# Kernel optimization log

Measured on AMD Instinct MI355X. Metric: run time of the kernel, lower is better.

The kernel has to match this reference:

```python
import jax, jax.numpy as jnp
import numpy as np

B, N, D = 2, 8192, 2
CIN, COUT = 6, 3
WID = 64
DEPTH = 3
M1, M2 = 12, 12
G = 64            # latent grid is G x G
K = 16            # neighbors
EDGE_IN = WID + 3 * D + 1  # 71


def _gelu(x):
    return jax.nn.gelu(x, approximate=False)  # torch nn.GELU default = exact erf


def _mlp1(x, W1, b1, W2, b2):
    # MLP(depth=1): Linear -> GELU -> Linear
    return _gelu(x @ W1 + b1) @ W2 + b2


def _mlp2(x, W1, b1, W2, b2, W3, b3):
    # MLP(depth=2): Linear -> GELU -> Linear -> GELU -> Linear
    h = _gelu(x @ W1 + b1)
    h = _gelu(h @ W2 + b2)
    return h @ W3 + b3


def _local_integral(src_c, qry_c, src_f, W1, b1, W2, b2, W3, b3):
    # src_c (B,Ns,D), qry_c (B,Nq,D), src_f (B,Ns,C) -> (B,Nq,WID)
    d2 = (jnp.sum(qry_c * qry_c, -1)[:, :, None]
          + jnp.sum(src_c * src_c, -1)[:, None, :]
          - 2.0 * jnp.einsum('bmd,bnd->bmn', qry_c, src_c))
    dist = jnp.sqrt(jnp.clip(d2, 0.0))                    # (B,Nq,Ns)
    neg, idx = jax.lax.top_k(-dist, K)                    # ascending distances
    nn_dist = -neg                                        # (B,Nq,K)
    gather = jax.vmap(lambda a, i: a[i])
    nc = gather(src_c, idx)                               # (B,Nq,K,D)
    nf = gather(src_f, idx)                               # (B,Nq,K,C)
    q = jnp.broadcast_to(qry_c[:, :, None, :], nc.shape)  # (B,Nq,K,D)
    rel = q - nc
    edge = jnp.concatenate([q, nc, rel, nn_dist[..., None], nf], axis=-1)
    # sigma = lower median of farthest-neighbor distance (torch.median semantics)
    last = jnp.sort(nn_dist[..., -1].reshape(-1))
    sigma = jnp.maximum(last[(last.shape[0] - 1) // 2], 1e-6)
    w = jnp.exp(-nn_dist[..., None] / sigma)              # (B,Nq,K,1)
    v = _mlp2(edge, W1, b1, W2, b2, W3, b3)               # (B,Nq,K,WID)
    return jnp.sum(w * v, axis=2) / jnp.clip(jnp.sum(w, axis=2), 1e-6)


def _spectral2d(x, w1, w2):
    # x (B,C,H,W); w* real-packed complex weights (Ci,Co,M1,M2,2)
    Bx, _, H, W = x.shape
    xf = jnp.fft.rfft2(x)                                 # (B,C,H,W//2+1) complex
    W1c = w1[..., 0] + 1j * w1[..., 1]
    W2c = w2[..., 0] + 1j * w2[..., 1]
    out = jnp.zeros((Bx, W1c.shape[1], H, W // 2 + 1), jnp.complex64)
    out = out.at[:, :, :M1, :M2].set(jnp.einsum('bixy,ioxy->boxy', xf[:, :, :M1, :M2], W1c))
    out = out.at[:, :, -M1:, :M2].set(jnp.einsum('bixy,ioxy->boxy', xf[:, :, -M1:, :M2], W2c))
    return jnp.fft.irfft2(out, s=(H, W))


def _fno_block(x, w1, w2, pw_W, pw_b):
    y = _spectral2d(x, w1, w2) + jnp.einsum('bihw,oi->bohw', x, pw_W) + pw_b[None, :, None, None]
    mu = jnp.mean(y, axis=(-2, -1), keepdims=True)        # InstanceNorm2d, no affine
    var = jnp.var(y, axis=(-2, -1), keepdims=True)
    return _gelu((y - mu) / jnp.sqrt(var + 1e-5))


def _latent_grid():
    ax = jnp.linspace(-1.0, 1.0, G, dtype=jnp.float32)
    gx, gy = jnp.meshgrid(ax, ax, indexing='ij')
    return jnp.stack([gx, gy], axis=-1).reshape(1, G * G, D)


def setup_inputs() -> dict:
    key = jax.random.key(0)
    ks = jax.random.split(key, 32)
    u = lambda k, sh, s: jax.random.uniform(k, sh, jnp.float32, -s, s)
    inp = {
        'coords': 2.0 * jax.random.uniform(ks[0], (B, N, D), jnp.float32) - 1.0,
        'features': jax.random.normal(ks[1], (B, N, CIN), jnp.float32),
        'lift_W1': u(ks[2], (CIN, WID), CIN ** -0.5), 'lift_b1': jnp.zeros((WID,), jnp.float32),
        'lift_W2': u(ks[3], (WID, WID), WID ** -0.5), 'lift_b2': jnp.zeros((WID,), jnp.float32),
        'gin_W1': u(ks[4], (EDGE_IN, WID), EDGE_IN ** -0.5), 'gin_b1': jnp.zeros((WID,), jnp.float32),
        'gin_W2': u(ks[5], (WID, WID), WID ** -0.5), 'gin_b2': jnp.zeros((WID,), jnp.float32),
        'gin_W3': u(ks[6], (WID, WID), WID ** -0.5), 'gin_b3': jnp.zeros((WID,), jnp.float32),
        'spec1': (1.0 / (WID * WID)) * jax.random.uniform(ks[7], (DEPTH, WID, WID, M1, M2, 2), jnp.float32),
        'spec2': (1.0 / (WID * WID)) * jax.random.uniform(ks[8], (DEPTH, WID, WID, M1, M2, 2), jnp.float32),
        'pw_W': u(ks[9], (DEPTH, WID, WID), WID ** -0.5),
        'pw_b': jnp.zeros((DEPTH, WID), jnp.float32),
        'gout_W1': u(ks[10], (EDGE_IN, WID), EDGE_IN ** -0.5), 'gout_b1': jnp.zeros((WID,), jnp.float32),
        'gout_W2': u(ks[11], (WID, WID), WID ** -0.5), 'gout_b2': jnp.zeros((WID,), jnp.float32),
        'gout_W3': u(ks[12], (WID, WID), WID ** -0.5), 'gout_b3': jnp.zeros((WID,), jnp.float32),
        'proj_W1': u(ks[13], (WID, WID), WID ** -0.5), 'proj_b1': jnp.zeros((WID,), jnp.float32),
        'proj_W2': u(ks[14], (WID, COUT), WID ** -0.5), 'proj_b2': jnp.zeros((COUT,), jnp.float32),
    }
    return inp


def reference(coords, features, lift_W1, lift_b1, lift_W2, lift_b2,
              gin_W1, gin_b1, gin_W2, gin_b2, gin_W3, gin_b3,
              spec1, spec2, pw_W, pw_b,
              gout_W1, gout_b1, gout_W2, gout_b2, gout_W3, gout_b3,
              proj_W1, proj_b1, proj_W2, proj_b2):
    grid = jnp.broadcast_to(_latent_grid(), (coords.shape[0], G * G, D))
    # lift node features
    feat = _mlp1(features, lift_W1, lift_b1, lift_W2, lift_b2)          # (B,N,WID)
    # GNO: points -> latent grid
    g = _local_integral(coords, grid, feat, gin_W1, gin_b1, gin_W2, gin_b2, gin_W3, gin_b3)
    x = g.reshape(-1, G, G, WID).transpose(0, 3, 1, 2)                  # (B,WID,G,G)
    for d in range(DEPTH):
        x = _fno_block(x, spec1[d], spec2[d], pw_W[d], pw_b[d])
    g = x.transpose(0, 2, 3, 1).reshape(-1, G * G, WID)                 # (B,G*G,WID)
    # GNO: latent grid -> points
    y = _local_integral(grid, coords, g, gout_W1, gout_b1, gout_W2, gout_b2, gout_W3, gout_b3)
    return _mlp1(y, proj_W1, proj_b1, proj_W2, proj_b2)                 # (B,N,COUT)
```

## Files before the change

kernel.cpp:

```cpp
#include <hip/hip_runtime.h>
#include <math.h>

#define B_ 2
#define N_ 8192
#define G_ 64
#define NG 4096
#define WID_ 64
#define K_ 16
#define CIN_ 6
#define COUT_ 3
#define PI_ 3.14159265358979323846

typedef unsigned long long u64k;
typedef __attribute__((ext_vector_type(8))) short bf16x8;
typedef __attribute__((ext_vector_type(16))) float f32x16;

__device__ __forceinline__ float gelu_f(float x) {
    float u = fabsf(x) * 0.70710678118654752440f;
    float t = __builtin_amdgcn_rcpf(fmaf(0.3275911f, u, 1.0f));
    float p = fmaf(fmaf(fmaf(fmaf(1.061405429f, t, -1.453152027f), t, 1.421413741f),
                        t, -0.284496736f), t, 0.254829592f) * t;
    float e = __expf(-u * u);
    float erfc_u = p * e;
    float phi = (x >= 0.f) ? fmaf(-0.5f, erfc_u, 1.0f) : (0.5f * erfc_u);
    return x * phi;
}
__device__ __forceinline__ int cellof(float v) {
    int c = (int)floorf((v + 1.0f) * 32.0f);
    return min(63, max(0, c));
}
__device__ __forceinline__ u64k umin64(u64k a, u64k b) { return a < b ? a : b; }
__device__ __forceinline__ u64k umax64(u64k a, u64k b) { return a < b ? b : a; }
__device__ __forceinline__ u64k shflxor64(u64k v, int m) {
    return (u64k)__shfl_xor((long long)v, m, 64);
}
__device__ __forceinline__ void bsort64(u64k& key, int lane) {
#pragma unroll
    for (int sz = 2; sz <= 64; sz <<= 1) {
#pragma unroll
        for (int j = sz >> 1; j >= 1; j >>= 1) {
            u64k o = shflxor64(key, j);
            bool keep_min = ((lane & j) == 0) == ((lane & sz) == 0);
            key = keep_min ? umin64(key, o) : umax64(key, o);
        }
    }
}
__device__ __forceinline__ void bmerge_into(u64k& R, u64k key, int lane) {
    u64k o = shflxor64(key, 63);
    u64k L = umin64(R, o);
#pragma unroll
    for (int j = 32; j >= 1; j >>= 1) {
        u64k t = shflxor64(L, j);
        L = ((lane & j) == 0) ? umin64(L, t) : umax64(L, t);
    }
    R = L;
}
__device__ __forceinline__ void cvt8v(float4 a, float4 b, bf16x8& hv, bf16x8& lv) {
    float v[8] = {a.x, a.y, a.z, a.w, b.x, b.y, b.z, b.w};
#pragma unroll
    for (int i = 0; i < 8; i++) {
        unsigned u = __float_as_uint(v[i]);
        unsigned r = (u + 0x8000u) & 0xffff0000u;
        hv[i] = (short)(r >> 16);
        float lo = v[i] - __uint_as_float(r);
        lv[i] = (short)(__float_as_uint(lo) >> 16);
    }
}
__device__ __forceinline__ bf16x8 ldfrag(const short* __restrict__ WB, int f, int lane) {
    return *(const bf16x8*)(WB + ((long)f * 64 + lane) * 8);
}
struct Frag4 { bf16x8 h0, l0, h1, l1; };
__device__ __forceinline__ Frag4 ldfrag4(const short* __restrict__ WB, int base, int nk,
                                         int kc, int lane) {
    Frag4 f;
    f.h0 = ldfrag(WB, base + (0 * nk + kc) * 2 + 0, lane);
    f.l0 = ldfrag(WB, base + (0 * nk + kc) * 2 + 1, lane);
    f.h1 = ldfrag(WB, base + (1 * nk + kc) * 2 + 0, lane);
    f.l1 = ldfrag(WB, base + (1 * nk + kc) * 2 + 1, lane);
    return f;
}

__global__ void __launch_bounds__(256) k_prep(
    const float* __restrict__ fin, const float* __restrict__ lW1,
    const float* __restrict__ lb1, const float* __restrict__ lW2,
    const float* __restrict__ lb2, float* __restrict__ fout,
    const float* __restrict__ W1a, const float* __restrict__ W2a,
    const float* __restrict__ W3a, short* __restrict__ WBa,
    const float* __restrict__ W1b, const float* __restrict__ W2b,
    const float* __restrict__ W3b, short* __restrict__ WBb,
    float4* __restrict__ gp, int* __restrict__ bins) {
    __shared__ float xr[4][8];
    __shared__ __align__(16) float h[4][64];
    int blk = blockIdx.x;
    if (blk < 4096) {
        int ql = threadIdx.x >> 6, j = threadIdx.x & 63;
        int node = blk * 4 + ql;
        if (j < CIN_) xr[ql][j] = fin[node * CIN_ + j];
        __syncthreads();
        float a = lb1[j];
#pragma unroll
        for (int i = 0; i < CIN_; i++) a = fmaf(xr[ql][i], lW1[i * 64 + j], a);
        h[ql][j] = gelu_f(a);
        __syncthreads();
        float a2 = lb2[j];
        for (int k = 0; k < 64; k += 4) {
            float w0 = lW2[(k + 0) * 64 + j], w1 = lW2[(k + 1) * 64 + j];
            float w2 = lW2[(k + 2) * 64 + j], w3 = lW2[(k + 3) * 64 + j];
            const float4 hv = *(const float4*)&h[ql][k];
            a2 = fmaf(hv.x, w0, fmaf(hv.y, w1, fmaf(hv.z, w2, fmaf(hv.w, w3, a2))));
        }
        fout[node * 64 + j] = a2;
    } else if (blk < 4122) {
        int t = (blk - 4096) * 256 + threadIdx.x;
        if (t >= 6656) return;
        int setb = (t >= 3328);
        int tt = t - (setb ? 3328 : 0);
        const float* W1s = setb ? W1b : W1a;
        const float* W2s = setb ? W2b : W2a;
        const float* W3s = setb ? W3b : W3a;
        short* WB = setb ? WBb : WBa;
        int f = tt >> 6, lane = tt & 63;
        const float* W; int hh, nt, kc, l1 = 0;
        if (f < 20)      { W = W1s; int r = f;      hh = r & 1; r >>= 1; nt = r / 5; kc = r % 5; l1 = 1; }
        else if (f < 36) { W = W2s; int r = f - 20; hh = r & 1; r >>= 1; nt = r / 4; kc = r % 4; }
        else             { W = W3s; int r = f - 36; hh = r & 1; r >>= 1; nt = r / 4; kc = r % 4; }
        int col = nt * 32 + (lane & 31);
        bf16x8 out;
#pragma unroll
        for (int i = 0; i < 8; i++) {
            int k = kc * 16 + (lane >> 5) * 8 + i;
            float w = 0.f;
            if (l1) {
                if (k < 7) w = W[k * 64 + col];
                else if (k >= 8 && k < 72) w = W[(k - 1) * 64 + col];
            } else {
                w = W[k * 64 + col];
            }
            unsigned u = __float_as_uint(w);
            unsigned hi = (u + 0x7fffu + ((u >> 16) & 1u)) & 0xffff0000u;
            float lo = w - __uint_as_float(hi);
            unsigned ul = __float_as_uint(lo);
            unsigned lr = ul + 0x7fffu + ((ul >> 16) & 1u);
            out[i] = hh ? (short)(lr >> 16) : (short)(hi >> 16);
        }
        *(bf16x8*)(WB + ((long)f * 64 + lane) * 8) = out;
    } else if (blk < 4138) {
        int t = (blk - 4122) * 256 + threadIdx.x;
        int i = t >> 6, j = t & 63;
        double st = 2.0 / 63.0;
        float gx = (i == 63) ? 1.0f : (float)(-1.0 + st * (double)i);
        float gy = (j == 63) ? 1.0f : (float)(-1.0 + st * (double)j);
        float s2 = __fadd_rn(__fmul_rn(gx, gx), __fmul_rn(gy, gy));
        gp[t] = make_float4(gx, gy, s2, 0.f);
    } else {
        int t = (blk - 4138) * 256 + threadIdx.x;
        bins[t] = 0;
    }
}

__global__ void k_bincount(const float2* __restrict__ coords, int* __restrict__ cnt) {
    int t = blockIdx.x * blockDim.x + threadIdx.x;
    if (t >= B_ * N_) return;
    float2 c = coords[t];
    int b = t >> 13;
    int cell = cellof(c.x) * 64 + cellof(c.y);
    atomicAdd(&cnt[b * 4096 + cell], 1);
}
__global__ void k_binscan(const int* __restrict__ cnt, int* __restrict__ offs) {
    int b = blockIdx.x, t = threadIdx.x;
    __shared__ int part[16];
    int4 v = ((const int4*)(cnt + b * 4096))[t];
    int sum = v.x + v.y + v.z + v.w;
    int lane = t & 63, wv = t >> 6;
    int ws = sum;
#pragma unroll
    for (int o = 1; o < 64; o <<= 1) {
        int u = __shfl_up(ws, o, 64);
        if (lane >= o) ws += u;
    }
    if (lane == 63) part[wv] = ws;
    __syncthreads();
    int base = 0;
#pragma unroll
    for (int k = 0; k < 16; k++) base += (k < wv) ? part[k] : 0;
    int incl = base + ws, excl = incl - sum;
    int* ob = offs + b * 4097;
    ob[4 * t] = excl; ob[4 * t + 1] = excl + v.x;
    ob[4 * t + 2] = excl + v.x + v.y; ob[4 * t + 3] = excl + v.x + v.y + v.z;
    if (t == 1023) ob[4096] = incl;
}
__global__ void k_binscatter(const float2* __restrict__ coords, const int* __restrict__ offs,
                             int* __restrict__ fill, float4* __restrict__ srt) {
    int t = blockIdx.x * blockDim.x + threadIdx.x;
    if (t >= B_ * N_) return;
    float2 c = coords[t];
    int b = t >> 13, n = t & 8191;
    int cell = cellof(c.x) * 64 + cellof(c.y);
    int pos = offs[b * 4097 + cell] + atomicAdd(&fill[b * 4096 + cell], 1);
    float s2 = __fadd_rn(__fmul_rn(c.x, c.x), __fmul_rn(c.y, c.y));
    srt[b * N_ + pos] = make_float4(c.x, c.y, s2, __int_as_float(n));
}

__global__ void __launch_bounds__(256) k_knn(
    const float4* __restrict__ gp, const float4* __restrict__ srt,
    const int* __restrict__ offs, const float2* __restrict__ coords,
    int* __restrict__ oidx_in, float* __restrict__ odist_in, float* __restrict__ lastd_in,
    int* __restrict__ oidx_out, float* __restrict__ odist_out, float* __restrict__ lastd_out) {
    int lane = threadIdx.x & 63;
    if (blockIdx.x < 2048) {
        int w = (blockIdx.x * blockDim.x + threadIdx.x) >> 6;
        int b = w >> 12, p = w & 4095;
        float4 q = gp[p];
        float qx = q.x, qy = q.y, q2 = q.z;
        int cqx = cellof(qx), cqy = cellof(qy);
        const float4* S = srt + b * N_;
        const int* OF = offs + b * 4097;

        u64k R = ~0ull;
        u64k pend = ~0ull;
        int fill = 0;

        auto flush = [&]() {
            bsort64(pend, lane);
            bmerge_into(R, pend, lane);
            pend = ~0ull;
            fill = 0;
        };
        auto feed = [&](int s0, int s1) {
            int cnt = s1 - s0;
            while (cnt > 0) {
                int take = min(cnt, 64 - fill);
                int t = lane - fill;
                if (t >= 0 && t < take) {
                    float4 sp = S[s0 + t];
                    float dot = __fadd_rn(__fmul_rn(qx, sp.x), __fmul_rn(qy, sp.y));
                    float d2 = __fsub_rn(__fadd_rn(q2, sp.z), 2.0f * dot);
                    d2 = fmaxf(d2, 0.0f);
                    pend = ((u64k)__float_as_uint(d2) << 32) | (unsigned)__float_as_int(sp.w);
                }
                fill += take; s0 += take; cnt -= take;
                if (fill == 64) flush();
            }
        };

        {
            int xa = max(cqx - 2, 0), xb = min(cqx + 2, 63);
            int ya = max(cqy - 2, 0), yb = min(cqy + 2, 63);
            for (int cx = xa; cx <= xb; cx++) feed(OF[cx * 64 + ya], OF[cx * 64 + yb + 1]);
        }
        int r = 2;
        while (true) {
            if (fill) flush();
            u64k T = (u64k)__shfl((long long)R, 15, 64);
            float d16 = __uint_as_float((unsigned)(T >> 32));
            float bm = (float)r * 0.03125f;
            if (d16 < bm * bm - 1e-5f) break;
            if (cqx - r <= 0 && cqx + r >= 63 && cqy - r <= 0 && cqy + r >= 63) break;
            r++;
            int ya = max(cqy - r, 0), yb = min(cqy + r, 63);
            if (cqx - r >= 0)  { int c0 = (cqx - r) * 64; feed(OF[c0 + ya], OF[c0 + yb + 1]); }
            if (cqx + r <= 63) { int c0 = (cqx + r) * 64; feed(OF[c0 + ya], OF[c0 + yb + 1]); }
            int xa2 = max(cqx - r + 1, 0), xb2 = min(cqx + r - 1, 63);
            for (int cx = xa2; cx <= xb2; cx++) {
                if (cqy - r >= 0)  { int cc = cx * 64 + cqy - r; feed(OF[cc], OF[cc + 1]); }
                if (cqy + r <= 63) { int cc = cx * 64 + cqy + r; feed(OF[cc], OF[cc + 1]); }
            }
        }
        if (lane < 16) {
            float d2 = __uint_as_float((unsigned)(R >> 32));
            float d = sqrtf(d2);
            oidx_in[w * 16 + lane] = (int)(unsigned)(R & 0xffffffffu);
            odist_in[w * 16 + lane] = d;
            if (lane == 15) lastd_in[w] = d;
        }
    } else {
        int w = ((blockIdx.x - 2048) * blockDim.x + threadIdx.x) >> 6;
        float2 c = coords[w];
        float qx = c.x, qy = c.y;
        float q2 = __fadd_rn(__fmul_rn(qx, qx), __fmul_rn(qy, qy));
        int i0 = (int)floorf((qx + 1.0f) * 31.5f);
        int j0 = (int)floorf((qy + 1.0f) * 31.5f);
        int li = min(max(i0 - 3, 0), 56);
        int lj = min(max(j0 - 3, 0), 56);
        int p = (li + (lane >> 3)) * 64 + (lj + (lane & 7));
        float4 sp = gp[p];
        float dot = __fadd_rn(__fmul_rn(qx, sp.x), __fmul_rn(qy, sp.y));
        float d2 = fmaxf(__fsub_rn(__fadd_rn(q2, sp.z), 2.0f * dot), 0.0f);
        u64k key = ((u64k)__float_as_uint(d2) << 32) | (unsigned)p;
        bsort64(key, lane);
        if (lane < 16) {
            float dd = sqrtf(__uint_as_float((unsigned)(key >> 32)));
            oidx_out[w * 16 + lane] = (int)(unsigned)(key & 0xffffffffu);
            odist_out[w * 16 + lane] = dd;
            if (lane == 15) lastd_out[w] = dd;
        }
    }
}

__global__ void __launch_bounds__(1024) k_median2(
    const float* __restrict__ vin, const float* __restrict__ vout,
    float* __restrict__ sig_in, float* __restrict__ sig_out) {
    const float* vals = blockIdx.x ? vout : vin;
    int n = blockIdx.x ? (B_ * N_) : (B_ * NG);
    float* sig = blockIdx.x ? sig_out : sig_in;
    __shared__ int wred[2][16];
    int tid = threadIdx.x;
    int lane = tid & 63, wv = tid >> 6;
    int cnt_per = n >> 10;
    unsigned v[16];
    for (int i = 0; i < cnt_per; i++) v[i] = __float_as_uint(vals[tid + (i << 10)]);
    int r = (n - 1) >> 1;
    unsigned prefix = 0;
    for (int bit = 31; bit >= 0; bit--) {
        unsigned cand = prefix | (1u << bit);
        int c = 0;
        for (int i = 0; i < cnt_per; i++) c += (v[i] < cand) ? 1 : 0;
        for (int o = 32; o >= 1; o >>= 1) c += __shfl_down(c, o, 64);
        int buf = bit & 1;
        if (lane == 0) wred[buf][wv] = c;
        __syncthreads();
        int tot = 0;
#pragma unroll
        for (int k = 0; k < 16; k++) tot += wred[buf][k];
        prefix = (tot <= r) ? cand : prefix;
    }
    if (tid == 0) *sig = fmaxf(__uint_as_float(prefix), 1e-6f);
}

template <int MODE>
__global__ void __launch_bounds__(128, 4) k_edge_mfma(
    const int* __restrict__ idxb, const float* __restrict__ distb,
    const float* __restrict__ sigp,
    const float2* __restrict__ coords, const float4* __restrict__ gp,
    const float* __restrict__ feats, const short* __restrict__ WB,
    const float* __restrict__ b1, const float* __restrict__ b2,
    const float* __restrict__ b3,
    float* __restrict__ outb) {
    constexpr int QSH  = (MODE == 0) ? 12 : 13;
    constexpr int QMSK = (MODE == 0) ? 4095 : 8191;
    constexpr long SR  = (MODE == 0) ? 8192 : 4096;
    __shared__ float X[2][2432];
    const int tid = threadIdx.x, wv = tid >> 6, lane = tid & 63;
    const int r31 = lane & 31, g = lane >> 5;
    const int qbase = (blockIdx.x * 2 + wv) * 2;
    const float sig = *sigp;
    float* X_ = X[wv];

    Frag4 cur = ldfrag4(WB, 0, 5, 0, lane);

    int si = 0; float wt = 0.f;
    if (lane < 32) {
        int q = lane >> 4, e = lane & 15;
        int gq = qbase + q;
        int b = gq >> QSH, p = gq & QMSK;
        si = idxb[gq * 16 + e];
        float d = distb[gq * 16 + e];
        wt = __expf(-d / sig);
        float qx, qy, sx, sy;
        if (MODE == 0) {
            float4 gv = gp[p]; qx = gv.x; qy = gv.y;
            float2 cc = coords[(long)b * SR + si]; sx = cc.x; sy = cc.y;
        } else {
            float2 cc = coords[gq]; qx = cc.x; qy = cc.y;
            float4 gv = gp[si]; sx = gv.x; sy = gv.y;
        }
        float* row = X_ + lane * 76;
        *(float4*)row       = make_float4(qx, qy, sx, sy);
        *(float4*)(row + 4) = make_float4(qx - sx, qy - sy, d, 0.f);
    }
    float swt = wt;
#pragma unroll
    for (int m = 1; m < 16; m <<= 1) swt += __shfl_xor(swt, m, 64);
    {
        float4 fv[8];
#pragma unroll
        for (int it = 0; it < 8; it++) {
            int slot = it * 64 + lane;
            int row = slot >> 4, f4 = slot & 15;
            int gq = qbase + (row >> 4);
            int b = gq >> QSH;
            int sr = __shfl(si, row, 64);
            fv[it] = *(const float4*)&feats[((long)b * SR + sr) * 64 + f4 * 4];
        }
#pragma unroll
        for (int it = 0; it < 8; it++) {
            int slot = it * 64 + lane;
            int row = slot >> 4, f4 = slot & 15;
            *(float4*)&X_[row * 76 + 8 + f4 * 4] = fv[it];
        }
    }

    f32x16 acc0, acc1;
    float4 xa, xb;
    {
        float bb0 = b1[r31], bb1 = b1[32 + r31];
#pragma unroll
        for (int i = 0; i < 16; i++) { acc0[i] = bb0; acc1[i] = bb1; }
        {
            const float* xp = &X_[r31 * 76 + g * 8];
            xa = *(const float4*)xp; xb = *(const float4*)(xp + 4);
        }
#pragma unroll
        for (int kc = 0; kc < 5; kc++) {
            Frag4 nxt = (kc < 4) ? ldfrag4(WB, 0, 5, kc + 1, lane)
                                 : ldfrag4(WB, 20, 4, 0, lane);
            bf16x8 ah, al;
            if (kc == 4 && g) {
#pragma unroll
                for (int i = 0; i < 8; i++) { ah[i] = 0; al[i] = 0; }
            } else {
                cvt8v(xa, xb, ah, al);
            }
            if (kc < 4 && (kc != 3 || g == 0)) {
                const float* xp = &X_[r31 * 76 + (kc + 1) * 16 + g * 8];
                xa = *(const float4*)xp; xb = *(const float4*)(xp + 4);
            }
            __builtin_amdgcn_s_setprio(1);
            acc0 = __builtin_amdgcn_mfma_f32_32x32x16_bf16(ah, cur.h0, acc0, 0, 0, 0);
            acc1 = __builtin_amdgcn_mfma_f32_32x32x16_bf16(ah, cur.h1, acc1, 0, 0, 0);
            acc0 = __builtin_amdgcn_mfma_f32_32x32x16_bf16(al, cur.h0, acc0, 0, 0, 0);
            acc1 = __builtin_amdgcn_mfma_f32_32x32x16_bf16(al, cur.h1, acc1, 0, 0, 0);
            acc0 = __builtin_amdgcn_mfma_f32_32x32x16_bf16(ah, cur.l0, acc0, 0, 0, 0);
            acc1 = __builtin_amdgcn_mfma_f32_32x32x16_bf16(ah, cur.l1, acc1, 0, 0, 0);
            __builtin_amdgcn_s_setprio(0);
            cur = nxt;
        }
    }
#pragma unroll
    for (int reg = 0; reg < 16; reg++) {
        int row = (reg & 3) + 8 * (reg >> 2) + 4 * g;
        X_[row * 76 + r31]      = gelu_f(acc0[reg]);
        X_[row * 76 + 32 + r31] = gelu_f(acc1[reg]);
    }
    {
        float bb0 = b2[r31], bb1 = b2[32 + r31];
#pragma unroll
        for (int i = 0; i < 16; i++) { acc0[i] = bb0; acc1[i] = bb1; }
        {
            const float* xp = &X_[r31 * 76 + g * 8];
            xa = *(const float4*)xp; xb = *(const float4*)(xp + 4);
        }
#pragma unroll
        for (int kc = 0; kc < 4; kc++) {
            Frag4 nxt = (kc < 3) ? ldfrag4(WB, 20, 4, kc + 1, lane)
                                 : ldfrag4(WB, 36, 4, 0, lane);
            bf16x8 ah, al;
            cvt8v(xa, xb, ah, al);
            if (kc < 3) {
                const float* xp = &X_[r31 * 76 + (kc + 1) * 16 + g * 8];
                xa = *(const float4*)xp; xb = *(const float4*)(xp + 4);
            }
            __builtin_amdgcn_s_setprio(1);
            acc0 = __builtin_amdgcn_mfma_f32_32x32x16_bf16(ah, cur.h0, acc0, 0, 0, 0);
            acc1 = __builtin_amdgcn_mfma_f32_32x32x16_bf16(ah, cur.h1, acc1, 0, 0, 0);
            acc0 = __builtin_amdgcn_mfma_f32_32x32x16_bf16(al, cur.h0, acc0, 0, 0, 0);
            acc1 = __builtin_amdgcn_mfma_f32_32x32x16_bf16(al, cur.h1, acc1, 0, 0, 0);
            acc0 = __builtin_amdgcn_mfma_f32_32x32x16_bf16(ah, cur.l0, acc0, 0, 0, 0);
            acc1 = __builtin_amdgcn_mfma_f32_32x32x16_bf16(ah, cur.l1, acc1, 0, 0, 0);
            __builtin_amdgcn_s_setprio(0);
            cur = nxt;
        }
    }
#pragma unroll
    for (int reg = 0; reg < 16; reg++) {
        int row = (reg & 3) + 8 * (reg >> 2) + 4 * g;
        X_[row * 76 + r31]      = gelu_f(acc0[reg]);
        X_[row * 76 + 32 + r31] = gelu_f(acc1[reg]);
    }
    {
        float bb0 = b3[r31], bb1 = b3[32 + r31];
#pragma unroll
        for (int i = 0; i < 16; i++) { acc0[i] = bb0; acc1[i] = bb1; }
        {
            const float* xp = &X_[r31 * 76 + g * 8];
            xa = *(const float4*)xp; xb = *(const float4*)(xp + 4);
        }
#pragma unroll
        for (int kc = 0; kc < 4; kc++) {
            Frag4 nxt = cur;
            if (kc < 3) nxt = ldfrag4(WB, 36, 4, kc + 1, lane);
            bf16x8 ah, al;
            cvt8v(xa, xb, ah, al);
            if (kc < 3) {
                const float* xp = &X_[r31 * 76 + (kc + 1) * 16 + g * 8];
                xa = *(const float4*)xp; xb = *(const float4*)(xp + 4);
            }
            __builtin_amdgcn_s_setprio(1);
            acc0 = __builtin_amdgcn_mfma_f32_32x32x16_bf16(ah, cur.h0, acc0, 0, 0, 0);
            acc1 = __builtin_amdgcn_mfma_f32_32x32x16_bf16(ah, cur.h1, acc1, 0, 0, 0);
            acc0 = __builtin_amdgcn_mfma_f32_32x32x16_bf16(al, cur.h0, acc0, 0, 0, 0);
            acc1 = __builtin_amdgcn_mfma_f32_32x32x16_bf16(al, cur.h1, acc1, 0, 0, 0);
            acc0 = __builtin_amdgcn_mfma_f32_32x32x16_bf16(ah, cur.l0, acc0, 0, 0, 0);
            acc1 = __builtin_amdgcn_mfma_f32_32x32x16_bf16(ah, cur.l1, acc1, 0, 0, 0);
            __builtin_amdgcn_s_setprio(0);
            cur = nxt;
        }
    }
    float wtv[16];
#pragma unroll
    for (int reg = 0; reg < 16; reg++)
        wtv[reg] = __shfl(wt, (reg & 3) + 8 * (reg >> 2) + 4 * g, 64);
    float s00 = 0.f, s01 = 0.f, s10 = 0.f, s11 = 0.f;
#pragma unroll
    for (int reg = 0; reg < 16; reg++) {
        if (reg < 8) { s00 = fmaf(wtv[reg], acc0[reg], s00); s01 = fmaf(wtv[reg], acc1[reg], s01); }
        else         { s10 = fmaf(wtv[reg], acc0[reg], s10); s11 = fmaf(wtv[reg], acc1[reg], s11); }
    }
    s00 += __shfl_xor(s00, 32, 64);
    s01 += __shfl_xor(s01, 32, 64);
    s10 += __shfl_xor(s10, 32, 64);
    s11 += __shfl_xor(s11, 32, 64);
    float sw0 = __shfl(swt, 0, 64), sw1 = __shfl(swt, 16, 64);
    if (g == 0) {
        float i0 = 1.0f / fmaxf(sw0, 1e-6f), i1 = 1.0f / fmaxf(sw1, 1e-6f);
        int gq0 = qbase, gq1 = qbase + 1;
        if (MODE == 0) {
            int b0 = gq0 >> QSH, p0 = gq0 & QMSK;
            int b1i = gq1 >> QSH, p1 = gq1 & QMSK;
            outb[((long)b0 * 64 + r31) * 4096 + p0]        = s00 * i0;
            outb[((long)b0 * 64 + 32 + r31) * 4096 + p0]   = s01 * i0;
            outb[((long)b1i * 64 + r31) * 4096 + p1]       = s10 * i1;
            outb[((long)b1i * 64 + 32 + r31) * 4096 + p1]  = s11 * i1;
        } else {
            outb[(long)gq0 * 64 + r31]      = s00 * i0;
            outb[(long)gq0 * 64 + 32 + r31] = s01 * i0;
            outb[(long)gq1 * 64 + r31]      = s10 * i1;
            outb[(long)gq1 * 64 + 32 + r31] = s11 * i1;
        }
    }
}

__global__ void k_transp(const float* __restrict__ src, float* __restrict__ dst, int R, int C) {
    __shared__ float t[32][33];
    int b = blockIdx.z;
    int c0 = blockIdx.x * 32, r0 = blockIdx.y * 32;
    int tx = threadIdx.x, ty0 = threadIdx.y;
    for (int yy = ty0; yy < 32; yy += 8) {
        int r = r0 + yy, c = c0 + tx;
        if (r < R && c < C) t[yy][tx] = src[((long)b * R + r) * C + c];
    }
    __syncthreads();
    for (int yy = ty0; yy < 32; yy += 8) {
        int c = c0 + yy, r = r0 + tx;
        if (r < R && c < C) dst[((long)b * C + c) * R + r] = t[tx][yy];
    }
}

__global__ void __launch_bounds__(384) k_f1(const float* __restrict__ x, float* __restrict__ Xh) {
    int blk = blockIdx.x >> 1;
    int chalf = blockIdx.x & 1;
    int tid = threadIdx.x;
    __shared__ __align__(16) float img[4096];
    __shared__ float Tre[64][6], Tim[64][6];
    __shared__ float cs[64], sn[64];
    if (tid < 64) {
        double a = (2.0 * PI_ / 64.0) * (double)tid;
        cs[tid] = (float)cos(a);
        sn[tid] = (float)sin(a);
    }
    for (int t = tid; t < 1024; t += 384)
        ((float4*)img)[t] = ((const float4*)(x + (long)blk * 4096))[t];
    __syncthreads();
    {
        int h = tid / 6, cl = tid - 6 * h;
        int c = chalf * 6 + cl;
        float cr = cs[c], sr = sn[c];
        float pr = 1.f, pi = 0.f;
        float re = 0.f, im = 0.f;
#pragma unroll 16
        for (int w = 0; w < 64; w++) {
            if (w == 32) {
                int k = (c * 32) & 63;
                pr = cs[k]; pi = sn[k];
            }
            float v = img[h * 64 + w];
            re = fmaf(v, pr, re);
            im = fmaf(-v, pi, im);
            float nr = pr * cr - pi * sr;
            pi = fmaf(pr, sr, pi * cr);
            pr = nr;
        }
        Tre[h][cl] = re; Tim[h][cl] = im;
    }
    __syncthreads();
    if (tid < 144) {
        int xx = tid / 6, cl = tid - 6 * xx;
        int r = (xx < 12) ? xx : (xx + 40);
        float cr = cs[r], sr = sn[r];
        float pr = 1.f, pi = 0.f;
        float re = 0.f, im = 0.f;
#pragma unroll 16
        for (int h = 0; h < 64; h++) {
            if (h == 32) {
                int k = (r * 32) & 63;
                pr = cs[k]; pi = sn[k];
            }
            float a = Tre[h][cl], bb = Tim[h][cl];
            re += a * pr + bb * pi;
            im += bb * pr - a * pi;
            float nr = pr * cr - pi * sr;
            pi = fmaf(pr, sr, pi * cr);
            pr = nr;
        }
        int m = xx * 12 + chalf * 6 + cl;
        Xh[((long)blk * 288 + m) * 2] = re;
        Xh[((long)blk * 288 + m) * 2 + 1] = im;
    }
}

__global__ void __launch_bounds__(320) k_f2(const float* __restrict__ Xh, const float* __restrict__ s1,
                                            const float* __restrict__ s2, float* __restrict__ Yh) {
    int bo = blockIdx.x;
    int b = bo >> 6, o = bo & 63;
    int m = threadIdx.x;
    if (m >= 288) return;
    int xx = m / 12, y = m - 12 * xx;
    const float* W; int xw;
    if (xx < 12) { W = s1; xw = xx; } else { W = s2; xw = xx - 12; }
    long wbase = (long)o * 288 + xw * 24 + y * 2;
    const float* Xb = Xh + ((long)b * 64) * 576;
    float re = 0.f, im = 0.f;
    for (int i = 0; i < 64; i++) {
        float2 wv = *(const float2*)&W[(long)i * 18432 + wbase];
        float2 xv = *(const float2*)&Xb[(long)i * 576 + m * 2];
        re += xv.x * wv.x - xv.y * wv.y;
        im += xv.x * wv.y + xv.y * wv.x;
    }
    float* Yb = Yh + (((long)b * 64 + o) * 288 + m) * 2;
    Yb[0] = re; Yb[1] = im;
}

__global__ void __launch_bounds__(1024) k_f3(const float* __restrict__ Yh, const float* __restrict__ x,
                                             const float* __restrict__ pwW, const float* __restrict__ pwb,
                                             float* __restrict__ xo) {
    int blk = blockIdx.x;
    int b = blk >> 6, o = blk & 63;
    int tid = threadIdx.x;
    __shared__ float yre[288], yim[288];
    __shared__ float Qre[64][12], Qim[64][12];
    __shared__ float cs[64], sn[64];
    __shared__ float red[16];
    if (tid < 64) {
        double a = (2.0 * PI_ / 64.0) * (double)tid;
        cs[tid] = (float)cos(a);
        sn[tid] = (float)sin(a);
    }
    if (tid < 288) {
        yre[tid] = Yh[((long)blk * 288 + tid) * 2];
        yim[tid] = Yh[((long)blk * 288 + tid) * 2 + 1];
    }
    __syncthreads();
    if (tid < 768) {
        int h = tid / 12, c = tid - 12 * h;
        float re = 0.f, im = 0.f;
#pragma unroll
        for (int xx = 0; xx < 24; xx++) {
            int r = (xx < 12) ? xx : (xx + 40);
            int k = (r * h) & 63;
            float wr = cs[k], wi = sn[k];
            float a = yre[xx * 12 + c], bb = yim[xx * 12 + c];
            re += a * wr - bb * wi;
            im += a * wi + bb * wr;
        }
        Qre[h][c] = re * (1.0f / 64.0f);
        Qim[h][c] = im * (1.0f / 64.0f);
    }
    __syncthreads();
    float bias = pwb[o];
    int h = tid >> 4;
    int w0 = (tid & 15) * 4;
    float sp0, sp1, sp2, sp3;
    {
        float base = Qre[h][0];
        sp0 = sp1 = sp2 = sp3 = base;
#pragma unroll
        for (int c = 1; c < 12; c++) {
            float qr = Qre[h][c], qi = Qim[h][c];
            int k0 = (c * w0) & 63, k1 = (c * (w0 + 1)) & 63;
            int k2 = (c * (w0 + 2)) & 63, k3 = (c * (w0 + 3)) & 63;
            sp0 += 2.0f * (qr * cs[k0] - qi * sn[k0]);
            sp1 += 2.0f * (qr * cs[k1] - qi * sn[k1]);
            sp2 += 2.0f * (qr * cs[k2] - qi * sn[k2]);
            sp3 += 2.0f * (qr * cs[k3] - qi * sn[k3]);
        }
    }
    float a0 = sp0 * (1.0f / 64.0f) + bias;
    float a1 = sp1 * (1.0f / 64.0f) + bias;
    float a2 = sp2 * (1.0f / 64.0f) + bias;
    float a3 = sp3 * (1.0f / 64.0f) + bias;
    const float* xb = x + ((long)b * 64) * 4096 + tid * 4;
    for (int i = 0; i < 64; i++) {
        float wv = pwW[o * 64 + i];
        const float4 xv = *(const float4*)(xb + (long)i * 4096);
        a0 = fmaf(xv.x, wv, a0);
        a1 = fmaf(xv.y, wv, a1);
        a2 = fmaf(xv.z, wv, a2);
        a3 = fmaf(xv.w, wv, a3);
    }
    float ssum = a0 + a1 + a2 + a3;
#pragma unroll
    for (int m = 1; m < 64; m <<= 1) ssum += __shfl_xor(ssum, m, 64);
    if ((tid & 63) == 0) red[tid >> 6] = ssum;
    __syncthreads();
    float mu = 0.f;
#pragma unroll
    for (int k = 0; k < 16; k++) mu += red[k];
    mu *= (1.0f / 4096.0f);
    __syncthreads();
    float d0 = a0 - mu, d1 = a1 - mu, d2 = a2 - mu, d3 = a3 - mu;
    float sq = d0 * d0 + d1 * d1 + d2 * d2 + d3 * d3;
#pragma unroll
    for (int m = 1; m < 64; m <<= 1) sq += __shfl_xor(sq, m, 64);
    if ((tid & 63) == 0) red[tid >> 6] = sq;
    __syncthreads();
    float var = 0.f;
#pragma unroll
    for (int k = 0; k < 16; k++) var += red[k];
    var *= (1.0f / 4096.0f);
    float inv = 1.0f / sqrtf(var + 1e-5f);
    float4 ov = make_float4(gelu_f(d0 * inv), gelu_f(d1 * inv), gelu_f(d2 * inv), gelu_f(d3 * inv));
    *(float4*)&xo[(long)blk * 4096 + tid * 4] = ov;
}

__global__ void __launch_bounds__(256) k_proj(
    const float* __restrict__ y, const float* __restrict__ W1, const float* __restrict__ b1,
    const float* __restrict__ W2, const float* __restrict__ b2, float* __restrict__ out) {
    __shared__ __align__(16) float yr[4][64];
    __shared__ float h[4][64];
    int ql = threadIdx.x >> 6, j = threadIdx.x & 63;
    long node = (long)blockIdx.x * 4 + ql;
    yr[ql][j] = y[node * 64 + j];
    __syncthreads();
    float a = b1[j];
    for (int k = 0; k < 64; k += 4) {
        float w0 = W1[(k + 0) * 64 + j], w1 = W1[(k + 1) * 64 + j];
        float w2 = W1[(k + 2) * 64 + j], w3 = W1[(k + 3) * 64 + j];
        const float4 hv = *(const float4*)&yr[ql][k];
        a = fmaf(hv.x, w0, fmaf(hv.y, w1, fmaf(hv.z, w2, fmaf(hv.w, w3, a))));
    }
    h[ql][j] = gelu_f(a);
    __syncthreads();
    if (j < 3) {
        float a2 = b2[j];
        for (int k = 0; k < 64; k++) a2 = fmaf(h[ql][k], W2[k * 3 + j], a2);
        out[node * 3 + j] = a2;
    }
}

extern "C" void kernel_launch(void* const* d_in, const int* in_sizes, int n_in,
                              void* d_out, int out_size, void* d_ws, size_t ws_size,
                              hipStream_t stream) {
    (void)in_sizes; (void)n_in; (void)out_size; (void)ws_size;
    const float* coords   = (const float*)d_in[0];
    const float* features = (const float*)d_in[1];
    const float* lift_W1 = (const float*)d_in[2];
    const float* lift_b1 = (const float*)d_in[3];
    const float* lift_W2 = (const float*)d_in[4];
    const float* lift_b2 = (const float*)d_in[5];
    const float* gin_W1 = (const float*)d_in[6];
    const float* gin_b1 = (const float*)d_in[7];
    const float* gin_W2 = (const float*)d_in[8];
    const float* gin_b2 = (const float*)d_in[9];
    const float* gin_W3 = (const float*)d_in[10];
    const float* gin_b3 = (const float*)d_in[11];
    const float* spec1 = (const float*)d_in[12];
    const float* spec2 = (const float*)d_in[13];
    const float* pw_W  = (const float*)d_in[14];
    const float* pw_b  = (const float*)d_in[15];
    const float* gout_W1 = (const float*)d_in[16];
    const float* gout_b1 = (const float*)d_in[17];
    const float* gout_W2 = (const float*)d_in[18];
    const float* gout_b2 = (const float*)d_in[19];
    const float* gout_W3 = (const float*)d_in[20];
    const float* gout_b3 = (const float*)d_in[21];
    const float* proj_W1 = (const float*)d_in[22];
    const float* proj_b1 = (const float*)d_in[23];
    const float* proj_W2 = (const float*)d_in[24];
    const float* proj_b2 = (const float*)d_in[25];

    char* ws = (char*)d_ws;
    size_t off = 0;
    auto alloc = [&](size_t bytes) -> char* {
        char* p = ws + off;
        off = (off + bytes + 255) & ~(size_t)255;
        return p;
    };
    float4* grid_pack = (float4*)alloc((size_t)NG * 16);
    float*  feat      = (float*)alloc((size_t)B_ * N_ * 64 * 4);
    int*    bin_cnt   = (int*)alloc((size_t)B_ * 4096 * 4);
    int*    bin_fill  = (int*)alloc((size_t)B_ * 4096 * 4);
    int*    bin_off   = (int*)alloc((size_t)B_ * 4097 * 4);
    float4* srt       = (float4*)alloc((size_t)B_ * N_ * 16);
    int*    idx_in    = (int*)alloc((size_t)B_ * NG * 16 * 4);
    float*  dist_in   = (float*)alloc((size_t)B_ * NG * 16 * 4);
    float*  lastd_in  = (float*)alloc((size_t)B_ * NG * 4);
    float*  sig_in    = (float*)alloc(256);
    float*  xb0       = (float*)alloc((size_t)B_ * 64 * NG * 4);
    float*  xb1       = (float*)alloc((size_t)B_ * 64 * NG * 4);
    float*  Xh        = (float*)alloc((size_t)B_ * 64 * 288 * 2 * 4);
    float*  Yh        = (float*)alloc((size_t)B_ * 64 * 288 * 2 * 4);
    float*  g2        = (float*)alloc((size_t)B_ * NG * 64 * 4);
    int*    idx_out   = (int*)alloc((size_t)B_ * N_ * 16 * 4);
    float*  dist_out  = (float*)alloc((size_t)B_ * N_ * 16 * 4);
    float*  lastd_out = (float*)alloc((size_t)B_ * N_ * 4);
    float*  sig_out   = (float*)alloc(256);
    float*  ybuf      = (float*)alloc((size_t)B_ * N_ * 64 * 4);
    short*  wb_in     = (short*)alloc((size_t)52 * 1024);
    short*  wb_out    = (short*)alloc((size_t)52 * 1024);

    k_prep<<<4202, 256, 0, stream>>>(features, lift_W1, lift_b1, lift_W2, lift_b2, feat,
                                     gin_W1, gin_W2, gin_W3, wb_in,
                                     gout_W1, gout_W2, gout_W3, wb_out,
                                     grid_pack, bin_cnt);
    k_bincount<<<(B_ * N_) / 256, 256, 0, stream>>>((const float2*)coords, bin_cnt);
    k_binscan<<<B_, 1024, 0, stream>>>(bin_cnt, bin_off);
    k_binscatter<<<(B_ * N_) / 256, 256, 0, stream>>>((const float2*)coords, bin_off, bin_fill, srt);
    k_knn<<<2048 + 4096, 256, 0, stream>>>(grid_pack, srt, bin_off, (const float2*)coords,
                                           idx_in, dist_in, lastd_in,
                                           idx_out, dist_out, lastd_out);
    k_median2<<<2, 1024, 0, stream>>>(lastd_in, lastd_out, sig_in, sig_out);
    k_edge_mfma<0><<<(B_ * NG) / 4, 128, 0, stream>>>(idx_in, dist_in, sig_in,
        (const float2*)coords, grid_pack, feat, wb_in,
        gin_b1, gin_b2, gin_b3, xb0);
    float* xc = xb0; float* xn = xb1;
    for (int d = 0; d < 3; d++) {
        k_f1<<<B_ * 64 * 2, 384, 0, stream>>>(xc, Xh);
        k_f2<<<B_ * 64, 320, 0, stream>>>(Xh, spec1 + (size_t)d * 1179648, spec2 + (size_t)d * 1179648, Yh);
        k_f3<<<B_ * 64, 1024, 0, stream>>>(Yh, xc, pw_W + (size_t)d * 4096, pw_b + (size_t)d * 64, xn);
        float* tmp = xc; xc = xn; xn = tmp;
    }
    {
        dim3 g(NG / 32, 64 / 32, B_); dim3 t(32, 8);
        k_transp<<<g, t, 0, stream>>>(xc, g2, 64, NG);
    }
    k_edge_mfma<1><<<(B_ * N_) / 4, 128, 0, stream>>>(idx_out, dist_out, sig_out,
        (const float2*)coords, grid_pack, g2, wb_out,
        gout_b1, gout_b2, gout_b3, ybuf);
    k_proj<<<(B_ * N_) / 4, 256, 0, stream>>>(ybuf, proj_W1, proj_b1, proj_W2, proj_b2, (float*)d_out);
}
```

Measured before the change: 363.0 us.

## Fuse spectral mixing, pointwise/norm and next-layer forward DFT; fold projection into edge kernel

Merges the spectral channel-mixing kernel into the inverse-DFT/pointwise kernel, splitting the 64-input-channel sum across two thread groups. For the first two FNO layers the same kernel also computes the next layer's truncated forward DFT from the result kept in shared memory, so the separate forward-DFT launch is needed only once. The output projection MLP moves into the epilogue of the second edge kernel, which removes the 64-wide intermediate buffer and one launch. The cost is much more shared memory per block and redundant weight loads in the fused kernels.

Result: faster. 336.9 us (median of 2 runs) (-7.2%).

```diff
diff --git a/kernel.cpp b/kernel.cpp
--- a/kernel.cpp
+++ b/kernel.cpp
@@ -335,6 +335,8 @@
     const float* __restrict__ feats, const short* __restrict__ WB,
     const float* __restrict__ b1, const float* __restrict__ b2,
     const float* __restrict__ b3,
+    const float* __restrict__ pW1, const float* __restrict__ pb1,
+    const float* __restrict__ pW2, const float* __restrict__ pb2,
     float* __restrict__ outb) {
     constexpr int QSH  = (MODE == 0) ? 12 : 13;
     constexpr int QMSK = (MODE == 0) ? 4095 : 8191;
@@ -511,21 +513,49 @@
     s10 += __shfl_xor(s10, 32, 64);
     s11 += __shfl_xor(s11, 32, 64);
     float sw0 = __shfl(swt, 0, 64), sw1 = __shfl(swt, 16, 64);
-    if (g == 0) {
-        float i0 = 1.0f / fmaxf(sw0, 1e-6f), i1 = 1.0f / fmaxf(sw1, 1e-6f);
-        int gq0 = qbase, gq1 = qbase + 1;
-        if (MODE == 0) {
+    float i0 = 1.0f / fmaxf(sw0, 1e-6f), i1 = 1.0f / fmaxf(sw1, 1e-6f);
+    int gq0 = qbase, gq1 = qbase + 1;
+    if (MODE == 0) {
+        if (g == 0) {
             int b0 = gq0 >> QSH, p0 = gq0 & QMSK;
             int b1i = gq1 >> QSH, p1 = gq1 & QMSK;
             outb[((long)b0 * 64 + r31) * 4096 + p0]        = s00 * i0;
             outb[((long)b0 * 64 + 32 + r31) * 4096 + p0]   = s01 * i0;
             outb[((long)b1i * 64 + r31) * 4096 + p1]       = s10 * i1;
             outb[((long)b1i * 64 + 32 + r31) * 4096 + p1]  = s11 * i1;
-        } else {
-            outb[(long)gq0 * 64 + r31]      = s00 * i0;
-            outb[(long)gq0 * 64 + 32 + r31] = s01 * i0;
-            outb[(long)gq1 * 64 + r31]      = s10 * i1;
-            outb[(long)gq1 * 64 + 32 + r31] = s11 * i1;
+        }
+    } else {
+        if (g == 0) {
+            X_[r31]       = s00 * i0;
+            X_[32 + r31]  = s01 * i0;
+            X_[64 + r31]  = s10 * i1;
+            X_[96 + r31]  = s11 * i1;
+        }
+        int j = lane;
+        float a0 = pb1[j], a1 = a0;
+        for (int k = 0; k < 64; k++) {
+            float w = pW1[k * 64 + j];
+            a0 = fmaf(X_[k], w, a0);
+            a1 = fmaf(X_[64 + k], w, a1);
+        }
+        float h0 = gelu_f(a0), h1 = gelu_f(a1);
+        float w20 = pW2[j * 3 + 0], w21 = pW2[j * 3 + 1], w22 = pW2[j * 3 + 2];
+        float p00 = h0 * w20, p01 = h0 * w21, p02 = h0 * w22;
+        float p10 = h1 * w20, p11 = h1 * w21, p12 = h1 * w22;
+#pragma unroll
+        for (int m = 1; m < 64; m <<= 1) {
+            p00 += __shfl_xor(p00, m, 64); p01 += __shfl_xor(p01, m, 64);
+            p02 += __shfl_xor(p02, m, 64);
+            p10 += __shfl_xor(p10, m, 64); p11 += __shfl_xor(p11, m, 64);
+            p12 += __shfl_xor(p12, m, 64);
+        }
+        if (lane == 0) {
+            outb[(long)gq0 * 3 + 0] = p00 + pb2[0];
+            outb[(long)gq0 * 3 + 1] = p01 + pb2[1];
+            outb[(long)gq0 * 3 + 2] = p02 + pb2[2];
+            outb[(long)gq1 * 3 + 0] = p10 + pb2[0];
+            outb[(long)gq1 * 3 + 1] = p11 + pb2[1];
+            outb[(long)gq1 * 3 + 2] = p12 + pb2[2];
         }
     }
 }
@@ -608,46 +638,48 @@
     }
 }
 
-__global__ void __launch_bounds__(320) k_f2(const float* __restrict__ Xh, const float* __restrict__ s1,
-                                            const float* __restrict__ s2, float* __restrict__ Yh) {
-    int bo = blockIdx.x;
-    int b = bo >> 6, o = bo & 63;
-    int m = threadIdx.x;
-    if (m >= 288) return;
-    int xx = m / 12, y = m - 12 * xx;
-    const float* W; int xw;
-    if (xx < 12) { W = s1; xw = xx; } else { W = s2; xw = xx - 12; }
-    long wbase = (long)o * 288 + xw * 24 + y * 2;
-    const float* Xb = Xh + ((long)b * 64) * 576;
-    float re = 0.f, im = 0.f;
-    for (int i = 0; i < 64; i++) {
-        float2 wv = *(const float2*)&W[(long)i * 18432 + wbase];
-        float2 xv = *(const float2*)&Xb[(long)i * 576 + m * 2];
-        re += xv.x * wv.x - xv.y * wv.y;
-        im += xv.x * wv.y + xv.y * wv.x;
-    }
-    float* Yb = Yh + (((long)b * 64 + o) * 288 + m) * 2;
-    Yb[0] = re; Yb[1] = im;
-}
-
-__global__ void __launch_bounds__(1024) k_f3(const float* __restrict__ Yh, const float* __restrict__ x,
-                                             const float* __restrict__ pwW, const float* __restrict__ pwb,
-                                             float* __restrict__ xo) {
+template <int RUN_DFT>
+__global__ void __launch_bounds__(1024) k_f23(
+    const float* __restrict__ Xh, const float* __restrict__ s1,
+    const float* __restrict__ s2, const float* __restrict__ x,
+    const float* __restrict__ pwW, const float* __restrict__ pwb,
+    float* __restrict__ xo, float* __restrict__ XhN) {
     int blk = blockIdx.x;
     int b = blk >> 6, o = blk & 63;
     int tid = threadIdx.x;
     __shared__ float yre[288], yim[288];
+    __shared__ float prr[576], pii[576];
     __shared__ float Qre[64][12], Qim[64][12];
     __shared__ float cs[64], sn[64];
     __shared__ float red[16];
+    __shared__ __align__(16) float img[4096];
+    __shared__ float Tre[64][12], Tim[64][12];
     if (tid < 64) {
         double a = (2.0 * PI_ / 64.0) * (double)tid;
         cs[tid] = (float)cos(a);
         sn[tid] = (float)sin(a);
     }
+    if (tid < 576) {
+        int grp = (tid >= 288) ? 1 : 0;
+        int m = tid - grp * 288;
+        int xx = m / 12, y = m - 12 * xx;
+        const float* W; int xw;
+        if (xx < 12) { W = s1; xw = xx; } else { W = s2; xw = xx - 12; }
+        long wbase = (long)o * 288 + xw * 24 + y * 2;
+        const float* Xb = Xh + ((long)b * 64) * 576;
+        float re = 0.f, im = 0.f;
+        for (int i = grp * 32; i < grp * 32 + 32; i++) {
+            float2 wv = *(const float2*)&W[(long)i * 18432 + wbase];
+            float2 xv = *(const float2*)&Xb[(long)i * 576 + m * 2];
+            re += xv.x * wv.x - xv.y * wv.y;
+            im += xv.x * wv.y + xv.y * wv.x;
+        }
+        prr[tid] = re; pii[tid] = im;
+    }
+    __syncthreads();
     if (tid < 288) {
-        yre[tid] = Yh[((long)blk * 288 + tid) * 2];
-        yim[tid] = Yh[((long)blk * 288 + tid) * 2 + 1];
+        yre[tid] = prr[tid] + prr[tid + 288];
+        yim[tid] = pii[tid] + pii[tid + 288];
     }
     __syncthreads();
     if (tid < 768) {
@@ -720,30 +752,52 @@
     float inv = 1.0f / sqrtf(var + 1e-5f);
     float4 ov = make_float4(gelu_f(d0 * inv), gelu_f(d1 * inv), gelu_f(d2 * inv), gelu_f(d3 * inv));
     *(float4*)&xo[(long)blk * 4096 + tid * 4] = ov;
-}
-
-__global__ void __launch_bounds__(256) k_proj(
-    const float* __restrict__ y, const float* __restrict__ W1, const float* __restrict__ b1,
-    const float* __restrict__ W2, const float* __restrict__ b2, float* __restrict__ out) {
-    __shared__ __align__(16) float yr[4][64];
-    __shared__ float h[4][64];
-    int ql = threadIdx.x >> 6, j = threadIdx.x & 63;
-    long node = (long)blockIdx.x * 4 + ql;
-    yr[ql][j] = y[node * 64 + j];
-    __syncthreads();
-    float a = b1[j];
-    for (int k = 0; k < 64; k += 4) {
-        float w0 = W1[(k + 0) * 64 + j], w1 = W1[(k + 1) * 64 + j];
-        float w2 = W1[(k + 2) * 64 + j], w3 = W1[(k + 3) * 64 + j];
-        const float4 hv = *(const float4*)&yr[ql][k];
-        a = fmaf(hv.x, w0, fmaf(hv.y, w1, fmaf(hv.z, w2, fmaf(hv.w, w3, a))));
-    }
-    h[ql][j] = gelu_f(a);
-    __syncthreads();
-    if (j < 3) {
-        float a2 = b2[j];
-        for (int k = 0; k < 64; k++) a2 = fmaf(h[ql][k], W2[k * 3 + j], a2);
-        out[node * 3 + j] = a2;
+    if (RUN_DFT) {
+        *(float4*)&img[tid * 4] = ov;
+        __syncthreads();
+        if (tid < 768) {
+            int hh = tid / 12, c = tid - 12 * hh;
+            float cr = cs[c], sr = sn[c];
+            float pr = 1.f, pi = 0.f;
+            float re = 0.f, im = 0.f;
+#pragma unroll 16
+            for (int w = 0; w < 64; w++) {
+                if (w == 32) {
+                    int k = (c * 32) & 63;
+                    pr = cs[k]; pi = sn[k];
+                }
+                float v = img[hh * 64 + w];
+                re = fmaf(v, pr, re);
+                im = fmaf(-v, pi, im);
+                float nr = pr * cr - pi * sr;
+                pi = fmaf(pr, sr, pi * cr);
+                pr = nr;
+            }
+            Tre[hh][c] = re; Tim[hh][c] = im;
+        }
+        __syncthreads();
+        if (tid < 288) {
+            int xx = tid / 12, cl = tid - 12 * xx;
+            int r = (xx < 12) ? xx : (xx + 40);
+            float cr = cs[r], sr = sn[r];
+            float pr = 1.f, pi = 0.f;
+            float re = 0.f, im = 0.f;
+#pragma unroll 16
+            for (int hh = 0; hh < 64; hh++) {
+                if (hh == 32) {
+                    int k = (r * 32) & 63;
+                    pr = cs[k]; pi = sn[k];
+                }
+                float a = Tre[hh][cl], bb = Tim[hh][cl];
+                re += a * pr + bb * pi;
+                im += bb * pr - a * pi;
+                float nr = pr * cr - pi * sr;
+                pi = fmaf(pr, sr, pi * cr);
+                pr = nr;
+            }
+            XhN[((long)blk * 288 + tid) * 2] = re;
+            XhN[((long)blk * 288 + tid) * 2 + 1] = im;
+        }
     }
 }
 
@@ -798,13 +852,12 @@
     float*  xb0       = (float*)alloc((size_t)B_ * 64 * NG * 4);
     float*  xb1       = (float*)alloc((size_t)B_ * 64 * NG * 4);
     float*  Xh        = (float*)alloc((size_t)B_ * 64 * 288 * 2 * 4);
-    float*  Yh        = (float*)alloc((size_t)B_ * 64 * 288 * 2 * 4);
+    float*  Xh2       = (float*)alloc((size_t)B_ * 64 * 288 * 2 * 4);
     float*  g2        = (float*)alloc((size_t)B_ * NG * 64 * 4);
     int*    idx_out   = (int*)alloc((size_t)B_ * N_ * 16 * 4);
     float*  dist_out  = (float*)alloc((size_t)B_ * N_ * 16 * 4);
     float*  lastd_out = (float*)alloc((size_t)B_ * N_ * 4);
     float*  sig_out   = (float*)alloc(256);
-    float*  ybuf      = (float*)alloc((size_t)B_ * N_ * 64 * 4);
     short*  wb_in     = (short*)alloc((size_t)52 * 1024);
     short*  wb_out    = (short*)alloc((size_t)52 * 1024);
 
@@ -821,20 +874,19 @@
     k_median2<<<2, 1024, 0, stream>>>(lastd_in, lastd_out, sig_in, sig_out);
     k_edge_mfma<0><<<(B_ * NG) / 4, 128, 0, stream>>>(idx_in, dist_in, sig_in,
         (const float2*)coords, grid_pack, feat, wb_in,
-        gin_b1, gin_b2, gin_b3, xb0);
-    float* xc = xb0; float* xn = xb1;
-    for (int d = 0; d < 3; d++) {
-        k_f1<<<B_ * 64 * 2, 384, 0, stream>>>(xc, Xh);
-        k_f2<<<B_ * 64, 320, 0, stream>>>(Xh, spec1 + (size_t)d * 1179648, spec2 + (size_t)d * 1179648, Yh);
-        k_f3<<<B_ * 64, 1024, 0, stream>>>(Yh, xc, pw_W + (size_t)d * 4096, pw_b + (size_t)d * 64, xn);
-        float* tmp = xc; xc = xn; xn = tmp;
-    }
+        gin_b1, gin_b2, gin_b3, nullptr, nullptr, nullptr, nullptr, xb0);
+    k_f1<<<B_ * 64 * 2, 384, 0, stream>>>(xb0, Xh);
+    k_f23<1><<<B_ * 64, 1024, 0, stream>>>(Xh,  spec1,           spec2,           xb0,
+        pw_W,            pw_b,        xb1, Xh2);
+    k_f23<1><<<B_ * 64, 1024, 0, stream>>>(Xh2, spec1 + 1179648, spec2 + 1179648, xb1,
+        pw_W + 4096,     pw_b + 64,   xb0, Xh);
+    k_f23<0><<<B_ * 64, 1024, 0, stream>>>(Xh,  spec1 + 2359296, spec2 + 2359296, xb0,
+        pw_W + 8192,     pw_b + 128,  xb1, Xh2);
     {
         dim3 g(NG / 32, 64 / 32, B_); dim3 t(32, 8);
-        k_transp<<<g, t, 0, stream>>>(xc, g2, 64, NG);
+        k_transp<<<g, t, 0, stream>>>(xb1, g2, 64, NG);
     }
     k_edge_mfma<1><<<(B_ * N_) / 4, 128, 0, stream>>>(idx_out, dist_out, sig_out,
         (const float2*)coords, grid_pack, g2, wb_out,
-        gout_b1, gout_b2, gout_b3, ybuf);
-    k_proj<<<(B_ * N_) / 4, 256, 0, stream>>>(ybuf, proj_W1, proj_b1, proj_W2, proj_b2, (float*)d_out);
-}
+        gout_b1, gout_b2, gout_b3, proj_W1, proj_b1, proj_W2, proj_b2, (float*)d_out);
+}
```
